# Optimization experiments

Hardware: AMD Instinct MI355X
Metric: run time of the kernel (lower is better)

Reference implementation:

```python
import jax, jax.numpy as jnp
import numpy as np
import math

B, S, D, H = 2, 2048, 1024, 16
DK = D // H


def setup_inputs() -> dict:
    key = jax.random.key(0)
    ks = jax.random.split(key, 12)
    s = 0.02
    return {
        "query": jax.random.normal(ks[0], (B, S, D), jnp.float32),
        "key": jax.random.normal(ks[1], (B, S, D), jnp.float32),
        "value": jax.random.normal(ks[2], (B, S, D), jnp.float32),
        "mask": jnp.zeros((1, 1, S, S), jnp.float32),
        "Wq": jax.random.normal(ks[3], (D, D), jnp.float32) * s,
        "bq": jnp.zeros((D,), jnp.float32),
        "Wk": jax.random.normal(ks[4], (D, D), jnp.float32) * s,
        "bk": jnp.zeros((D,), jnp.float32),
        "Wv": jax.random.normal(ks[5], (D, D), jnp.float32) * s,
        "bv": jnp.zeros((D,), jnp.float32),
        "Wpost": jax.random.normal(ks[6], (D, D), jnp.float32) * s,
        "bpost": jnp.zeros((D,), jnp.float32),
        "per_dim_scale": jnp.zeros((DK,), jnp.float32),
    }


def reference(query, key, value, mask, Wq, bq, Wk, bk, Wv, bv, Wpost, bpost, per_dim_scale):
    # Linear projections (torch Linear: x @ W.T + b), split heads -> [B, H, S, DK]
    def proj(x, W, b):
        return (x @ W.T + b).reshape(B, S, H, DK).transpose(0, 2, 1, 3)

    q = proj(query, Wq, bq)
    k = proj(key, Wk, bk)
    v = proj(value, Wv, bv)

    # PerDimScale: scale = (1/ln2) / sqrt(d_k) * softplus(per_dim_scale)
    r_softplus_0 = 1.442695041
    scale = (r_softplus_0 / math.sqrt(DK)) * jax.nn.softplus(per_dim_scale)
    q = q * scale  # broadcast over last dim

    # Full attention matrix [B, H, S, S] + additive mask + softmax (dropout p=0)
    attn = jnp.einsum('bhqd,bhkd->bhqk', q, k) + mask
    attn = jax.nn.softmax(attn, axis=-1)

    out = jnp.einsum('bhqk,bhkd->bhqd', attn, v)
    out = out.transpose(0, 2, 1, 3).reshape(B, S, D)
    return out @ Wpost.T + bpost
```

## Files before the change

### kernel.cpp

```cpp
#include <hip/hip_runtime.h>
#include <math.h>

typedef __bf16 bf16;
typedef __bf16 bf16x8 __attribute__((ext_vector_type(8)));
typedef float f32x4 __attribute__((ext_vector_type(4)));

static constexpr int NB = 2, NS = 2048, ND = 1024, NH = 16, NDK = 64;
static constexpr float LOG2E = 1.442695041f;

__device__ __forceinline__ f32x4 mfma16(bf16x8 a, bf16x8 b, f32x4 c) {
  return __builtin_amdgcn_mfma_f32_16x16x32_bf16(a, b, c, 0, 0, 0);
}

__device__ __forceinline__ float exp2_fast(float x) {
  return __builtin_amdgcn_exp2f(x);
}

__device__ __forceinline__ void gload16(const void* g, void* l) {
  __builtin_amdgcn_global_load_lds(
      (const __attribute__((address_space(1))) void*)g,
      (__attribute__((address_space(3))) void*)l, 16, 0, 0);
}

__global__ __launch_bounds__(256) void cvt_bf16(
    const float* __restrict__ s0, const float* __restrict__ s1, const float* __restrict__ s2,
    const float* __restrict__ s3, const float* __restrict__ s4, const float* __restrict__ s5,
    const float* __restrict__ s6,
    bf16* __restrict__ d0, bf16* __restrict__ d1, bf16* __restrict__ d2,
    bf16* __restrict__ d3, bf16* __restrict__ d4, bf16* __restrict__ d5,
    bf16* __restrict__ d6, int n8x, int n8w,
    const float* __restrict__ pds, float* __restrict__ scale,
    const float* __restrict__ mask, int* __restrict__ flag, int n4) {
  const int y = blockIdx.y;
  if (y == 7) {
    if (blockIdx.x == 0 && threadIdx.x < NDK) {
      float x = pds[threadIdx.x];
      float sp = fmaxf(x, 0.0f) + log1pf(expf(-fabsf(x)));
      scale[threadIdx.x] = (LOG2E * LOG2E / 8.0f) * sp;
    }
    int idx = blockIdx.x * blockDim.x + threadIdx.x;
    int stride = 256 * blockDim.x;
    unsigned acc = 0;
    for (int i = idx; i < n4; i += stride) {
      float4 v = ((const float4*)mask)[i];
      acc |= (__float_as_uint(v.x) << 1) | (__float_as_uint(v.y) << 1)
           | (__float_as_uint(v.z) << 1) | (__float_as_uint(v.w) << 1);
    }
    if (acc != 0) atomicOr(flag, 1);
    return;
  }
  const float* s = y == 0 ? s0 : y == 1 ? s1 : y == 2 ? s2 : y == 3 ? s3
                 : y == 4 ? s4 : y == 5 ? s5 : s6;
  bf16* d = y == 0 ? d0 : y == 1 ? d1 : y == 2 ? d2 : y == 3 ? d3
          : y == 4 ? d4 : y == 5 ? d5 : d6;
  const int n8 = y < 3 ? n8x : n8w;
  for (int i = blockIdx.x * 256 + threadIdx.x; i < n8; i += gridDim.x * 256) {
    const float4* f = (const float4*)s + 2 * (size_t)i;
    float4 a = f[0], b = f[1];
    bf16x8 o;
    o[0] = (bf16)a.x; o[1] = (bf16)a.y; o[2] = (bf16)a.z; o[3] = (bf16)a.w;
    o[4] = (bf16)b.x; o[5] = (bf16)b.y; o[6] = (bf16)b.z; o[7] = (bf16)b.w;
    *((bf16x8*)d + i) = o;
  }
}

__global__ __launch_bounds__(256) void qkv_mm(
    const bf16* __restrict__ Xq, const bf16* __restrict__ Xk, const bf16* __restrict__ Xv,
    const bf16* __restrict__ Wqb, const bf16* __restrict__ Wkb, const bf16* __restrict__ Wvb,
    const float* __restrict__ bq, const float* __restrict__ bk, const float* __restrict__ bv,
    const float* __restrict__ scale2,
    bf16* __restrict__ Qs, bf16* __restrict__ Ks, bf16* __restrict__ Vt, int mode0) {
  __shared__ __align__(16) bf16 la[128 * 64];
  __shared__ __align__(16) bf16 lb[128 * 64];
  const int which = mode0 + blockIdx.y;
  const bf16* A  = which == 0 ? Xq  : which == 1 ? Xk  : Wvb;
  const bf16* Bm = which == 0 ? Wqb : which == 1 ? Wkb : Xv;
  const int t = threadIdx.x, lane = t & 63, wave = t >> 6;
  const int wm = wave >> 1, wn = wave & 1;
  int bm, bn;
  if (which == 2) { bm = blockIdx.x & 7; bn = blockIdx.x >> 3; }
  else            { bm = blockIdx.x >> 3; bn = blockIdx.x & 7; }
  const int g = lane >> 4, l15 = lane & 15;
  const int sr = wave * 8 + (lane >> 3);
  const int sc = ((lane & 7) ^ (lane >> 3)) * 8;
  const bf16* Abase = A  + (size_t)(bm * 128) * ND;
  const bf16* Bbase = Bm + (size_t)(bn * 128) * ND;

  f32x4 acc[4][4] = {};

  for (int kt = 0; kt < ND; kt += 64) {
    for (int c = 0; c < 4; ++c) {
      gload16(Abase + (size_t)(c * 32 + sr) * ND + kt + sc, la + c * 2048 + wave * 512);
      gload16(Bbase + (size_t)(c * 32 + sr) * ND + kt + sc, lb + c * 2048 + wave * 512);
    }
    __syncthreads();
    __builtin_amdgcn_s_setprio(1);
    for (int kk = 0; kk < 2; ++kk) {
      bf16x8 af[4], bfv[4];
      for (int m = 0; m < 4; ++m) {
        const int rr = wm * 64 + m * 16 + l15;
        af[m] = *(const bf16x8*)&la[rr * 64 + (((g + 4 * kk) ^ (rr & 7)) << 3)];
      }
      for (int n = 0; n < 4; ++n) {
        const int rr = wn * 64 + n * 16 + l15;
        bfv[n] = *(const bf16x8*)&lb[rr * 64 + (((g + 4 * kk) ^ (rr & 7)) << 3)];
      }
      for (int m = 0; m < 4; ++m)
        for (int n = 0; n < 4; ++n)
          acc[m][n] = mfma16(af[m], bfv[n], acc[m][n]);
    }
    __builtin_amdgcn_s_setprio(0);
    __syncthreads();
  }

  const int lr4 = g * 4;
  if (which != 2) {
    const float* bias = which ? bk : bq;
    bf16* outp = which ? Ks : Qs;
    for (int m = 0; m < 4; ++m) {
      const int grow0 = bm * 128 + wm * 64 + m * 16 + lr4;
      for (int n = 0; n < 4; ++n) {
        const int gcol = bn * 128 + wn * 64 + n * 16 + l15;
        const int h = gcol >> 6, dk = gcol & 63;
        const float bia = bias[gcol];
        const float sc2 = which ? 1.0f : scale2[dk];
        for (int r = 0; r < 4; ++r) {
          const int grow = grow0 + r;
          float v = acc[m][n][r] + bia;
          if (which == 0) v *= sc2;
          const int bb = grow >> 11, s = grow & (NS - 1);
          outp[(((size_t)(bb * NH + h)) * NS + s) * NDK + dk] = (bf16)v;
        }
      }
    }
  } else {
    for (int m = 0; m < 4; ++m) {
      const int d0 = bm * 128 + wm * 64 + m * 16 + lr4;
      for (int n = 0; n < 4; ++n) {
        const int gcol = bn * 128 + wn * 64 + n * 16 + l15;
        const int bb = gcol >> 11, s = gcol & (NS - 1);
        for (int r = 0; r < 4; ++r) {
          const int d = d0 + r;
          const float v = acc[m][n][r] + bv[d];
          const int h = d >> 6, dk = d & 63;
          Vt[(((size_t)(bb * NH + h)) * NDK + dk) * NS + s] = (bf16)v;
        }
      }
    }
  }
}

__global__ __launch_bounds__(256) void post_mm2(
    const bf16* __restrict__ A, const bf16* __restrict__ Bm,
    const float* __restrict__ bias, float* __restrict__ out) {
  __shared__ __align__(16) bf16 la[2][64 * 64];
  __shared__ __align__(16) bf16 lb[2][128 * 64];
  const int t = threadIdx.x, lane = t & 63, wave = t >> 6;
  const int bm = blockIdx.x >> 3, bn = blockIdx.x & 7;
  const int g = lane >> 4, l15 = lane & 15;
  const int sr = wave * 8 + (lane >> 3);
  const int sc = ((lane & 7) ^ (lane >> 3)) * 8;
  const bf16* Abase = A  + (size_t)(bm * 64) * ND;
  const bf16* Bbase = Bm + (size_t)(bn * 128) * ND;

  f32x4 acc[4][2] = {};

  auto stage = [&](int kt, int b) {
    for (int c = 0; c < 2; ++c)
      gload16(Abase + (size_t)(c * 32 + sr) * ND + kt + sc, la[b] + c * 2048 + wave * 512);
    for (int c = 0; c < 4; ++c)
      gload16(Bbase + (size_t)(c * 32 + sr) * ND + kt + sc, lb[b] + c * 2048 + wave * 512);
  };

  stage(0, 0);
  asm volatile("s_waitcnt vmcnt(0)" ::: "memory");
  __builtin_amdgcn_s_barrier();

  for (int it = 0; it < 16; ++it) {
    const int cur = it & 1;
    if (it + 1 < 16) stage((it + 1) * 64, cur ^ 1);

    __builtin_amdgcn_s_setprio(1);
    for (int kk = 0; kk < 2; ++kk) {
      bf16x8 af[4], bfv[2];
      for (int m = 0; m < 4; ++m) {
        const int rr = m * 16 + l15;
        af[m] = *(const bf16x8*)&la[cur][rr * 64 + (((g + 4 * kk) ^ (rr & 7)) << 3)];
      }
      for (int n = 0; n < 2; ++n) {
        const int rr = wave * 32 + n * 16 + l15;
        bfv[n] = *(const bf16x8*)&lb[cur][rr * 64 + (((g + 4 * kk) ^ (rr & 7)) << 3)];
      }
      for (int m = 0; m < 4; ++m)
        for (int n = 0; n < 2; ++n)
          acc[m][n] = mfma16(af[m], bfv[n], acc[m][n]);
    }
    __builtin_amdgcn_s_setprio(0);

    asm volatile("s_waitcnt vmcnt(0)" ::: "memory");
    __builtin_amdgcn_s_barrier();
  }

  for (int m = 0; m < 4; ++m) {
    const int grow0 = bm * 64 + m * 16 + g * 4;
    for (int n = 0; n < 2; ++n) {
      const int gcol = bn * 128 + wave * 32 + n * 16 + l15;
      const float bia = bias[gcol];
      for (int r = 0; r < 4; ++r)
        out[(size_t)(grow0 + r) * ND + gcol] = acc[m][n][r] + bia;
    }
  }
}

__global__ __launch_bounds__(512) void attn5(
    const bf16* __restrict__ Qs, const bf16* __restrict__ Ks,
    const bf16* __restrict__ Vt, const float* __restrict__ mask,
    const int* __restrict__ flag, bf16* __restrict__ Obs) {
  __shared__ __align__(16) bf16 lk[2 * 64 * 64];
  __shared__ __align__(16) bf16 lv[2 * 64 * 64];
  __shared__ __align__(16) bf16 lp[8 * 16 * 64];

  const int t = threadIdx.x, lane = t & 63, wave = t >> 6;
  const int g = lane >> 4, l15 = lane & 15;
  const int bh = blockIdx.y;
  const int qbase = blockIdx.x * 128 + wave * 16;
  const bool use_mask = (*flag) != 0;

  const bf16* Qh = Qs + (size_t)bh * NS * NDK;
  const bf16* Kh = Ks + (size_t)bh * NS * NDK;
  const bf16* Vh = Vt + (size_t)bh * NDK * NS;

  bf16x8 qf[2];
#pragma unroll
  for (int kk = 0; kk < 2; ++kk)
    qf[kk] = *(const bf16x8*)&Qh[(size_t)(qbase + l15) * NDK + kk * 32 + g * 8];

  f32x4 o_acc[4] = {};
  float lsum[4] = {0.0f, 0.0f, 0.0f, 0.0f};

  unsigned kfo[2][4];
#pragma unroll
  for (int kk = 0; kk < 2; ++kk)
#pragma unroll
    for (int n = 0; n < 4; ++n)
      kfo[kk][n] = (unsigned)((n * 16 + l15) * 64 + (((g + 4 * kk) ^ (l15 & 7)) << 3));
  unsigned pwo[4][4];
#pragma unroll
  for (int n = 0; n < 4; ++n)
#pragma unroll
    for (int r = 0; r < 4; ++r) {
      const int q = g * 4 + r;
      pwo[n][r] = (unsigned)(wave * 1024 + q * 64 + ((n * 16 + l15) ^ ((q & 7) << 3)));
    }
  unsigned pro[2];
#pragma unroll
  for (int kk = 0; kk < 2; ++kk)
    pro[kk] = (unsigned)(wave * 1024 + l15 * 64 + ((kk * 32 + g * 8) ^ ((l15 & 7) << 3)));

  const int srow = wave * 8 + (lane >> 3);
  const int sc = ((lane & 7) ^ (lane >> 3)) * 8;

  auto stage = [&](int kv, int b) {
    gload16(Kh + (size_t)(kv + srow) * NDK + sc, lk + b * 4096 + wave * 512);
    gload16(Vh + (size_t)srow * NS + kv + sc, lv + b * 4096 + wave * 512);
  };

  auto body = [&](int kv, int cur) {
    if (kv + 64 < NS) stage(kv + 64, cur ^ 1);

    f32x4 sacc[4] = {};
    __builtin_amdgcn_s_setprio(1);
#pragma unroll
    for (int kk = 0; kk < 2; ++kk)
#pragma unroll
      for (int n = 0; n < 4; ++n)
        sacc[n] = mfma16(qf[kk], *(const bf16x8*)&lk[cur * 4096 + kfo[kk][n]], sacc[n]);
    __builtin_amdgcn_s_setprio(0);

    if (use_mask) {
#pragma unroll
      for (int n = 0; n < 4; ++n)
#pragma unroll
        for (int r = 0; r < 4; ++r)
          sacc[n][r] += LOG2E * mask[(size_t)(qbase + g * 4 + r) * NS + kv + n * 16 + l15];
    }

#pragma unroll
    for (int n = 0; n < 4; ++n)
#pragma unroll
      for (int r = 0; r < 4; ++r) {
        const float e = exp2_fast(sacc[n][r]);
        lsum[r] += e;
        lp[pwo[n][r]] = (bf16)e;
      }

#pragma unroll
    for (int kk = 0; kk < 2; ++kk) {
      const bf16x8 pf = *(const bf16x8*)&lp[pro[kk]];
      __builtin_amdgcn_s_setprio(1);
#pragma unroll
      for (int n = 0; n < 4; ++n)
        o_acc[n] = mfma16(pf, *(const bf16x8*)&lv[cur * 4096 + kfo[kk][n]], o_acc[n]);
      __builtin_amdgcn_s_setprio(0);
    }

    asm volatile("s_waitcnt vmcnt(0)" ::: "memory");
    __builtin_amdgcn_s_barrier();
  };

  stage(0, 0);
  asm volatile("s_waitcnt vmcnt(0)" ::: "memory");
  __builtin_amdgcn_s_barrier();

  for (int kv = 0; kv < NS; kv += 128) {
    body(kv, 0);
    body(kv + 64, 1);
  }

  const int bidx = bh >> 4, h = bh & 15;
#pragma unroll
  for (int r = 0; r < 4; ++r) {
    float rs = lsum[r];
    rs += __shfl_xor(rs, 1, 64);
    rs += __shfl_xor(rs, 2, 64);
    rs += __shfl_xor(rs, 4, 64);
    rs += __shfl_xor(rs, 8, 64);
    const float rinv = 1.0f / rs;
    const int qrow = qbase + g * 4 + r;
#pragma unroll
    for (int n = 0; n < 4; ++n)
      Obs[((size_t)(bidx * NS + qrow)) * ND + h * 64 + n * 16 + l15] = (bf16)(o_acc[n][r] * rinv);
  }
}

extern "C" void kernel_launch(void* const* d_in, const int* in_sizes, int n_in,
                              void* d_out, int out_size, void* d_ws, size_t ws_size,
                              hipStream_t stream) {
  (void)in_sizes; (void)n_in; (void)out_size;
  const float* query = (const float*)d_in[0];
  const float* key   = (const float*)d_in[1];
  const float* value = (const float*)d_in[2];
  const float* mask  = (const float*)d_in[3];
  const float* Wq    = (const float*)d_in[4];
  const float* bq    = (const float*)d_in[5];
  const float* Wk    = (const float*)d_in[6];
  const float* bk    = (const float*)d_in[7];
  const float* Wv    = (const float*)d_in[8];
  const float* bv    = (const float*)d_in[9];
  const float* Wpost = (const float*)d_in[10];
  const float* bpost = (const float*)d_in[11];
  const float* pds   = (const float*)d_in[12];

  char* ws = (char*)d_ws;
  const size_t MB = 1u << 20;
  bf16* Xq  = (bf16*)(ws + 0 * MB);
  bf16* Xk  = (bf16*)(ws + 8 * MB);
  bf16* Xv  = (bf16*)(ws + 16 * MB);
  bf16* Wqb = (bf16*)(ws + 24 * MB);
  bf16* Wkb = (bf16*)(ws + 26 * MB);
  bf16* Wvb = (bf16*)(ws + 28 * MB);
  bf16* Wpb = (bf16*)(ws + 30 * MB);
  float* scale2 = (float*)(ws + 32 * MB);
  int* flag     = (int*)(ws + 32 * MB + 256);

  const bool fused = ws_size >= (size_t)50 * MB;
  bf16 *Qsp, *Ksp, *Vtp, *Obsp;
  if (fused) {
    Qsp = (bf16*)d_out;
    Ksp = (bf16*)((char*)d_out + 8 * MB);
    Vtp = (bf16*)(ws + 33 * MB);
    Obsp = (bf16*)(ws + 41 * MB);
  } else {
    Qsp = (bf16*)d_out;
    Ksp = Xq;
    Vtp = Xk;
    Obsp = Xv;
  }

  (void)hipMemsetAsync(flag, 0, sizeof(int), stream);

  cvt_bf16<<<dim3(256, 8), 256, 0, stream>>>(query, key, value, Wq, Wk, Wv, Wpost,
                                             Xq, Xk, Xv, Wqb, Wkb, Wvb, Wpb,
                                             NB * NS * ND / 8, ND * ND / 8,
                                             pds, scale2, mask, flag, NS * NS / 4);

  if (fused) {
    qkv_mm<<<dim3(256, 3), 256, 0, stream>>>(Xq, Xk, Xv, Wqb, Wkb, Wvb,
                                             bq, bk, bv, scale2, Qsp, Ksp, Vtp, 0);
  } else {
    qkv_mm<<<dim3(256, 1), 256, 0, stream>>>(Xq, Xk, Xv, Wqb, Wkb, Wvb,
                                             bq, bk, bv, scale2, Qsp, Ksp, Vtp, 0);
    qkv_mm<<<dim3(256, 1), 256, 0, stream>>>(Xq, Xk, Xv, Wqb, Wkb, Wvb,
                                             bq, bk, bv, scale2, Qsp, Ksp, Vtp, 1);
    qkv_mm<<<dim3(256, 1), 256, 0, stream>>>(Xq, Xk, Xv, Wqb, Wkb, Wvb,
                                             bq, bk, bv, scale2, Qsp, Ksp, Vtp, 2);
  }

  attn5<<<dim3(16, 32), 512, 0, stream>>>(Qsp, Ksp, Vtp, mask, flag, Obsp);

  post_mm2<<<512, 256, 0, stream>>>(Obsp, Wpb, bpost, (float*)d_out);
}
```

Measured before the change: 133.0 us.

## Fuse activation bf16 conversion into QKV GEMM and transpose attention score layout

Result: slower. 147.7 us (+11.1%).

```diff
diff --git a/kernel.cpp b/kernel.cpp
--- a/kernel.cpp
+++ b/kernel.cpp
@@ -2,6 +2,7 @@
 #include <math.h>
 
 typedef __bf16 bf16;
+typedef __bf16 bf16x4 __attribute__((ext_vector_type(4)));
 typedef __bf16 bf16x8 __attribute__((ext_vector_type(8)));
 typedef float f32x4 __attribute__((ext_vector_type(4)));
 
@@ -22,17 +23,15 @@
       (__attribute__((address_space(3))) void*)l, 16, 0, 0);
 }
 
-__global__ __launch_bounds__(256) void cvt_bf16(
-    const float* __restrict__ s0, const float* __restrict__ s1, const float* __restrict__ s2,
-    const float* __restrict__ s3, const float* __restrict__ s4, const float* __restrict__ s5,
-    const float* __restrict__ s6,
-    bf16* __restrict__ d0, bf16* __restrict__ d1, bf16* __restrict__ d2,
-    bf16* __restrict__ d3, bf16* __restrict__ d4, bf16* __restrict__ d5,
-    bf16* __restrict__ d6, int n8x, int n8w,
+__global__ __launch_bounds__(256) void cvtw_prep(
+    const float* __restrict__ s0, const float* __restrict__ s1,
+    const float* __restrict__ s2, const float* __restrict__ s3,
+    bf16* __restrict__ d0, bf16* __restrict__ d1,
+    bf16* __restrict__ d2, bf16* __restrict__ d3, int n8w,
     const float* __restrict__ pds, float* __restrict__ scale,
     const float* __restrict__ mask, int* __restrict__ flag, int n4) {
   const int y = blockIdx.y;
-  if (y == 7) {
+  if (y == 4) {
     if (blockIdx.x == 0 && threadIdx.x < NDK) {
       float x = pds[threadIdx.x];
       float sp = fmaxf(x, 0.0f) + log1pf(expf(-fabsf(x)));
@@ -49,12 +48,9 @@
     if (acc != 0) atomicOr(flag, 1);
     return;
   }
-  const float* s = y == 0 ? s0 : y == 1 ? s1 : y == 2 ? s2 : y == 3 ? s3
-                 : y == 4 ? s4 : y == 5 ? s5 : s6;
-  bf16* d = y == 0 ? d0 : y == 1 ? d1 : y == 2 ? d2 : y == 3 ? d3
-          : y == 4 ? d4 : y == 5 ? d5 : d6;
-  const int n8 = y < 3 ? n8x : n8w;
-  for (int i = blockIdx.x * 256 + threadIdx.x; i < n8; i += gridDim.x * 256) {
+  const float* s = y == 0 ? s0 : y == 1 ? s1 : y == 2 ? s2 : s3;
+  bf16* d = y == 0 ? d0 : y == 1 ? d1 : y == 2 ? d2 : d3;
+  for (int i = blockIdx.x * 256 + threadIdx.x; i < n8w; i += gridDim.x * 256) {
     const float4* f = (const float4*)s + 2 * (size_t)i;
     float4 a = f[0], b = f[1];
     bf16x8 o;
@@ -65,7 +61,7 @@
 }
 
 __global__ __launch_bounds__(256) void qkv_mm(
-    const bf16* __restrict__ Xq, const bf16* __restrict__ Xk, const bf16* __restrict__ Xv,
+    const float* __restrict__ Xqf, const float* __restrict__ Xkf, const float* __restrict__ Xvf,
     const bf16* __restrict__ Wqb, const bf16* __restrict__ Wkb, const bf16* __restrict__ Wvb,
     const float* __restrict__ bq, const float* __restrict__ bk, const float* __restrict__ bv,
     const float* __restrict__ scale2,
@@ -73,8 +69,6 @@
   __shared__ __align__(16) bf16 la[128 * 64];
   __shared__ __align__(16) bf16 lb[128 * 64];
   const int which = mode0 + blockIdx.y;
-  const bf16* A  = which == 0 ? Xq  : which == 1 ? Xk  : Wvb;
-  const bf16* Bm = which == 0 ? Wqb : which == 1 ? Wkb : Xv;
   const int t = threadIdx.x, lane = t & 63, wave = t >> 6;
   const int wm = wave >> 1, wn = wave & 1;
   int bm, bn;
@@ -83,15 +77,27 @@
   const int g = lane >> 4, l15 = lane & 15;
   const int sr = wave * 8 + (lane >> 3);
   const int sc = ((lane & 7) ^ (lane >> 3)) * 8;
-  const bf16* Abase = A  + (size_t)(bm * 128) * ND;
-  const bf16* Bbase = Bm + (size_t)(bn * 128) * ND;
+
+  const float* Xf = which == 0 ? Xqf : which == 1 ? Xkf : Xvf;
+  const float* Xbase = Xf + (size_t)((which == 2 ? bn : bm) * 128) * ND;
+  const bf16* Wb = which == 0 ? Wqb : which == 1 ? Wkb : Wvb;
+  const bf16* Wbase = Wb + (size_t)((which == 2 ? bm : bn) * 128) * ND;
+  bf16* ldsX = (which == 2) ? lb : la;
+  bf16* ldsW = (which == 2) ? la : lb;
 
   f32x4 acc[4][4] = {};
 
   for (int kt = 0; kt < ND; kt += 64) {
+    for (int c = 0; c < 4; ++c)
+      gload16(Wbase + (size_t)(c * 32 + sr) * ND + kt + sc, ldsW + c * 2048 + wave * 512);
     for (int c = 0; c < 4; ++c) {
-      gload16(Abase + (size_t)(c * 32 + sr) * ND + kt + sc, la + c * 2048 + wave * 512);
-      gload16(Bbase + (size_t)(c * 32 + sr) * ND + kt + sc, lb + c * 2048 + wave * 512);
+      const float* gp = Xbase + (size_t)(c * 32 + sr) * ND + kt + sc;
+      float4 a0 = *(const float4*)gp;
+      float4 a1 = *(const float4*)(gp + 4);
+      bf16x8 o;
+      o[0] = (bf16)a0.x; o[1] = (bf16)a0.y; o[2] = (bf16)a0.z; o[3] = (bf16)a0.w;
+      o[4] = (bf16)a1.x; o[5] = (bf16)a1.y; o[6] = (bf16)a1.z; o[7] = (bf16)a1.w;
+      *(bf16x8*)(ldsX + c * 2048 + wave * 512 + lane * 8) = o;
     }
     __syncthreads();
     __builtin_amdgcn_s_setprio(1);
@@ -212,7 +218,7 @@
   }
 }
 
-__global__ __launch_bounds__(512) void attn5(
+__global__ __launch_bounds__(512) void attn10(
     const bf16* __restrict__ Qs, const bf16* __restrict__ Ks,
     const bf16* __restrict__ Vt, const float* __restrict__ mask,
     const int* __restrict__ flag, bf16* __restrict__ Obs) {
@@ -236,7 +242,7 @@
     qf[kk] = *(const bf16x8*)&Qh[(size_t)(qbase + l15) * NDK + kk * 32 + g * 8];
 
   f32x4 o_acc[4] = {};
-  float lsum[4] = {0.0f, 0.0f, 0.0f, 0.0f};
+  float lsum = 0.0f;
 
   unsigned kfo[2][4];
 #pragma unroll
@@ -244,14 +250,10 @@
 #pragma unroll
     for (int n = 0; n < 4; ++n)
       kfo[kk][n] = (unsigned)((n * 16 + l15) * 64 + (((g + 4 * kk) ^ (l15 & 7)) << 3));
-  unsigned pwo[4][4];
+  unsigned pw4[4];
 #pragma unroll
   for (int n = 0; n < 4; ++n)
-#pragma unroll
-    for (int r = 0; r < 4; ++r) {
-      const int q = g * 4 + r;
-      pwo[n][r] = (unsigned)(wave * 1024 + q * 64 + ((n * 16 + l15) ^ ((q & 7) << 3)));
-    }
+    pw4[n] = (unsigned)(wave * 1024 + l15 * 64 + ((n * 16 + g * 4) ^ ((l15 & 7) << 3)));
   unsigned pro[2];
 #pragma unroll
   for (int kk = 0; kk < 2; ++kk)
@@ -274,7 +276,7 @@
     for (int kk = 0; kk < 2; ++kk)
 #pragma unroll
       for (int n = 0; n < 4; ++n)
-        sacc[n] = mfma16(qf[kk], *(const bf16x8*)&lk[cur * 4096 + kfo[kk][n]], sacc[n]);
+        sacc[n] = mfma16(*(const bf16x8*)&lk[cur * 4096 + kfo[kk][n]], qf[kk], sacc[n]);
     __builtin_amdgcn_s_setprio(0);
 
     if (use_mask) {
@@ -282,17 +284,20 @@
       for (int n = 0; n < 4; ++n)
 #pragma unroll
         for (int r = 0; r < 4; ++r)
-          sacc[n][r] += LOG2E * mask[(size_t)(qbase + g * 4 + r) * NS + kv + n * 16 + l15];
-    }
-
-#pragma unroll
-    for (int n = 0; n < 4; ++n)
+          sacc[n][r] += LOG2E * mask[(size_t)(qbase + l15) * NS + kv + n * 16 + g * 4 + r];
+    }
+
+#pragma unroll
+    for (int n = 0; n < 4; ++n) {
+      bf16x4 pk;
 #pragma unroll
       for (int r = 0; r < 4; ++r) {
         const float e = exp2_fast(sacc[n][r]);
-        lsum[r] += e;
-        lp[pwo[n][r]] = (bf16)e;
-      }
+        lsum += e;
+        pk[r] = (bf16)e;
+      }
+      *(bf16x4*)&lp[pw4[n]] = pk;
+    }
 
 #pragma unroll
     for (int kk = 0; kk < 2; ++kk) {
@@ -317,15 +322,14 @@
     body(kv + 64, 1);
   }
 
+  float rs = lsum;
+  rs += __shfl_xor(rs, 16, 64);
+  rs += __shfl_xor(rs, 32, 64);
   const int bidx = bh >> 4, h = bh & 15;
 #pragma unroll
   for (int r = 0; r < 4; ++r) {
-    float rs = lsum[r];
-    rs += __shfl_xor(rs, 1, 64);
-    rs += __shfl_xor(rs, 2, 64);
-    rs += __shfl_xor(rs, 4, 64);
-    rs += __shfl_xor(rs, 8, 64);
-    const float rinv = 1.0f / rs;
+    const float rsr = __shfl(rs, g * 4 + r, 64);
+    const float rinv = 1.0f / rsr;
     const int qrow = qbase + g * 4 + r;
 #pragma unroll
     for (int n = 0; n < 4; ++n)
@@ -353,9 +357,6 @@
 
   char* ws = (char*)d_ws;
   const size_t MB = 1u << 20;
-  bf16* Xq  = (bf16*)(ws + 0 * MB);
-  bf16* Xk  = (bf16*)(ws + 8 * MB);
-  bf16* Xv  = (bf16*)(ws + 16 * MB);
   bf16* Wqb = (bf16*)(ws + 24 * MB);
   bf16* Wkb = (bf16*)(ws + 26 * MB);
   bf16* Wvb = (bf16*)(ws + 28 * MB);
@@ -372,31 +373,30 @@
     Obsp = (bf16*)(ws + 41 * MB);
   } else {
     Qsp = (bf16*)d_out;
-    Ksp = Xq;
-    Vtp = Xk;
-    Obsp = Xv;
+    Ksp = (bf16*)(ws + 0 * MB);
+    Vtp = (bf16*)(ws + 8 * MB);
+    Obsp = (bf16*)(ws + 16 * MB);
   }
 
   (void)hipMemsetAsync(flag, 0, sizeof(int), stream);
 
-  cvt_bf16<<<dim3(256, 8), 256, 0, stream>>>(query, key, value, Wq, Wk, Wv, Wpost,
-                                             Xq, Xk, Xv, Wqb, Wkb, Wvb, Wpb,
-                                             NB * NS * ND / 8, ND * ND / 8,
-                                             pds, scale2, mask, flag, NS * NS / 4);
+  cvtw_prep<<<dim3(256, 5), 256, 0, stream>>>(Wq, Wk, Wv, Wpost,
+                                              Wqb, Wkb, Wvb, Wpb, ND * ND / 8,
+                                              pds, scale2, mask, flag, NS * NS / 4);
 
   if (fused) {
-    qkv_mm<<<dim3(256, 3), 256, 0, stream>>>(Xq, Xk, Xv, Wqb, Wkb, Wvb,
+    qkv_mm<<<dim3(256, 3), 256, 0, stream>>>(query, key, value, Wqb, Wkb, Wvb,
                                              bq, bk, bv, scale2, Qsp, Ksp, Vtp, 0);
   } else {
-    qkv_mm<<<dim3(256, 1), 256, 0, stream>>>(Xq, Xk, Xv, Wqb, Wkb, Wvb,
+    qkv_mm<<<dim3(256, 1), 256, 0, stream>>>(query, key, value, Wqb, Wkb, Wvb,
                                              bq, bk, bv, scale2, Qsp, Ksp, Vtp, 0);
-    qkv_mm<<<dim3(256, 1), 256, 0, stream>>>(Xq, Xk, Xv, Wqb, Wkb, Wvb,
+    qkv_mm<<<dim3(256, 1), 256, 0, stream>>>(query, key, value, Wqb, Wkb, Wvb,
                                              bq, bk, bv, scale2, Qsp, Ksp, Vtp, 1);
-    qkv_mm<<<dim3(256, 1), 256, 0, stream>>>(Xq, Xk, Xv, Wqb, Wkb, Wvb,
+    qkv_mm<<<dim3(256, 1), 256, 0, stream>>>(query, key, value, Wqb, Wkb, Wvb,
                                              bq, bk, bv, scale2, Qsp, Ksp, Vtp, 2);
   }
 
-  attn5<<<dim3(16, 32), 512, 0, stream>>>(Qsp, Ksp, Vtp, mask, flag, Obsp);
+  attn10<<<dim3(16, 32), 512, 0, stream>>>(Qsp, Ksp, Vtp, mask, flag, Obsp);
 
   post_mm2<<<512, 256, 0, stream>>>(Obsp, Wpb, bpost, (float*)d_out);
 }
```
